# Kernel tuning notes

Measured on AMD Instinct MI355X. Metric: run time of the kernel, lower is better.

Reference implementation:

```python
import jax, jax.numpy as jnp
import numpy as np

B, N = 8192, 512
WEIGHT_THRESHOLD = 0.0
EPS = 1e-5


def setup_inputs() -> dict:
    key = jax.random.key(0)
    k1, k2, k3 = jax.random.split(key, 3)
    src_points = jax.random.normal(k1, (B, N, 3), dtype=jnp.float32)
    tgt_points = jax.random.normal(k2, (B, N, 3), dtype=jnp.float32)
    weights = jax.random.uniform(k3, (B, N), dtype=jnp.float32)
    return {"src_points": src_points, "tgt_points": tgt_points, "weights": weights}


def _weighted_procrustes(src, tgt, w):
    # threshold + normalize weights  (B, N)
    w = jnp.where(w < WEIGHT_THRESHOLD, jnp.zeros_like(w), w)
    w = w / (jnp.sum(w, axis=1, keepdims=True) + EPS)
    w3 = w[..., None]                                   # (B, N, 1)
    # weighted centroids (B, 1, 3)
    src_c = jnp.sum(w3 * src, axis=1, keepdims=True)
    tgt_c = jnp.sum(w3 * tgt, axis=1, keepdims=True)
    src0 = src - src_c
    tgt0 = tgt - tgt_c
    # weighted covariance H = src0^T (w * tgt0)  -> (B, 3, 3)
    H = jnp.einsum("bni,bnj->bij", src0, w3 * tgt0)
    U, S, Vh = jnp.linalg.svd(H)
    V = jnp.swapaxes(Vh, -1, -2)
    Ut = jnp.swapaxes(U, -1, -2)
    # reflection correction: diag(1, 1, sign(det(V U^T)))
    det = jnp.linalg.det(jnp.matmul(V, Ut))             # (B,)
    ones = jnp.ones((src.shape[0], 2), dtype=src.dtype)
    d = jnp.concatenate([ones, jnp.sign(det)[:, None]], axis=1)  # (B, 3)
    R = jnp.einsum("bij,bj,bjk->bik", V, d, Ut)         # (B, 3, 3)
    t = tgt_c[:, 0, :] - jnp.einsum("bij,bj->bi", R, src_c[:, 0, :])  # (B, 3)
    return R, t


def reference(src_points, tgt_points, weights):
    return _weighted_procrustes(src_points, tgt_points, weights)
```

## Files before the change

### kernel.cpp

```cpp
#include <hip/hip_runtime.h>

#define NPTS 512
#define BLOCK 256
#define XPS 68

#define GLOBAL_AS(p) ((const __attribute__((address_space(1))) void*)(p))
#define LDS_AS(p)    ((__attribute__((address_space(3))) void*)(p))

__global__ __launch_bounds__(BLOCK) void wproc_moments(
    const float* __restrict__ src,
    const float* __restrict__ tgt,
    const float* __restrict__ wts,
    float* __restrict__ ws)
{
    const int b = blockIdx.x;
    const int t = threadIdx.x;
    const int wave = t >> 6, lane = t & 63;

    __shared__ __align__(16) char smem[4 * 16 * XPS * 4];
    __shared__ float red[4][16];

    const char* sb = (const char*)(src + (size_t)b * (NPTS * 3));
    const char* tb = (const char*)(tgt + (size_t)b * (NPTS * 3));
    const char* wb = (const char*)(wts + (size_t)b * NPTS);

    for (int c = wave; c < 14; c += 4) {
        const char* g;
        if (c < 6)       g = sb + (size_t)c * 1024;
        else if (c < 12) g = tb + (size_t)(c - 6) * 1024;
        else             g = wb + (size_t)(c - 12) * 1024;
        __builtin_amdgcn_global_load_lds(
            GLOBAL_AS(g + lane * 16),
            LDS_AS(smem + c * 1024),
            16, 0, 2);
    }
    __syncthreads();

    const float* s_s = (const float*)smem;
    const float* s_t = (const float*)(smem + 6144);
    const float* s_w = (const float*)(smem + 12288);

    float acc[16];
    #pragma unroll
    for (int i = 0; i < 16; ++i) acc[i] = 0.f;

    #pragma unroll
    for (int k = 0; k < 2; ++k) {
        const int p = t + k * 256;
        float w = s_w[p];
        w = (w < 0.f) ? 0.f : w;
        const float sx = s_s[3 * p + 0], sy = s_s[3 * p + 1], sz = s_s[3 * p + 2];
        const float tx = s_t[3 * p + 0], ty = s_t[3 * p + 1], tz = s_t[3 * p + 2];
        acc[0] += w;
        acc[1] += w * sx; acc[2] += w * sy; acc[3] += w * sz;
        acc[4] += w * tx; acc[5] += w * ty; acc[6] += w * tz;
        const float wsx = w * sx, wsy = w * sy, wsz = w * sz;
        acc[7]  += wsx * tx; acc[8]  += wsx * ty; acc[9]  += wsx * tz;
        acc[10] += wsy * tx; acc[11] += wsy * ty; acc[12] += wsy * tz;
        acc[13] += wsz * tx; acc[14] += wsz * ty; acc[15] += wsz * tz;
    }
    __syncthreads();

    float (*xp)[16][XPS] = (float (*)[16][XPS])smem;
    #pragma unroll
    for (int m = 0; m < 16; ++m) xp[wave][m][lane] = acc[m];

    {
        const int m = lane & 15, q = lane >> 4;
        const float4* row = (const float4*)&xp[wave][m][0] + 4 * q;
        float4 a0 = row[0], a1 = row[1], a2 = row[2], a3 = row[3];
        a0.x += a1.x; a0.y += a1.y; a0.z += a1.z; a0.w += a1.w;
        a2.x += a3.x; a2.y += a3.y; a2.z += a3.z; a2.w += a3.w;
        a0.x += a2.x; a0.y += a2.y; a0.z += a2.z; a0.w += a2.w;
        float v = (a0.x + a0.y) + (a0.z + a0.w);
        v += __shfl_xor(v, 16, 64);
        v += __shfl_xor(v, 32, 64);
        if (q == 0) red[wave][m] = v;
    }
    __syncthreads();

    if (t < 16) {
        ws[(size_t)b * 16 + t] =
            (red[0][t] + red[1][t]) + (red[2][t] + red[3][t]);
    }
}

__global__ __launch_bounds__(BLOCK) void wproc_solve(
    const float* __restrict__ ws,
    float* __restrict__ out,
    int B)
{
    const int b = blockIdx.x * BLOCK + threadIdx.x;
    if (b >= B) return;

    double m[16];
    #pragma unroll
    for (int i = 0; i < 16; ++i) m[i] = (double)ws[(size_t)b * 16 + i];

    const double T = m[0] + 1e-5;
    const double f = 2.0 - m[0] / T;
    const double cs[3] = { m[1] / T, m[2] / T, m[3] / T };
    const double ct[3] = { m[4] / T, m[5] / T, m[6] / T };
    double H[3][3];
    for (int i = 0; i < 3; ++i)
        for (int j = 0; j < 3; ++j)
            H[i][j] = m[7 + i * 3 + j] / T - f * cs[i] * ct[j];

    double A[3][3];
    for (int i = 0; i < 3; ++i)
        for (int j = 0; j < 3; ++j)
            A[i][j] = H[0][i] * H[0][j] + H[1][i] * H[1][j] + H[2][i] * H[2][j];

    double V[3][3] = { {1, 0, 0}, {0, 1, 0}, {0, 0, 1} };
    for (int sweep = 0; sweep < 5; ++sweep) {
        for (int pair = 0; pair < 3; ++pair) {
            const int p = (pair == 2) ? 1 : 0;
            const int q = (pair == 0) ? 1 : 2;
            const double apq = A[p][q];
            if (apq == 0.0) continue;
            const double theta = (A[q][q] - A[p][p]) / (2.0 * apq);
            const double tt = ((theta >= 0.0) ? 1.0 : -1.0)
                            / (fabs(theta) + sqrt(theta * theta + 1.0));
            const double c = 1.0 / sqrt(tt * tt + 1.0);
            const double sn = tt * c;
            for (int k = 0; k < 3; ++k) {
                const double akp = A[k][p], akq = A[k][q];
                A[k][p] = c * akp - sn * akq;
                A[k][q] = sn * akp + c * akq;
            }
            for (int k = 0; k < 3; ++k) {
                const double apk = A[p][k], aqk = A[q][k];
                A[p][k] = c * apk - sn * aqk;
                A[q][k] = sn * apk + c * aqk;
            }
            for (int k = 0; k < 3; ++k) {
                const double vkp = V[k][p], vkq = V[k][q];
                V[k][p] = c * vkp - sn * vkq;
                V[k][q] = sn * vkp + c * vkq;
            }
        }
    }

    const double lam[3] = { A[0][0], A[1][1], A[2][2] };
    int i0 = 0, i1 = 1, i2 = 2;
    if (lam[i0] < lam[i1]) { int tmp = i0; i0 = i1; i1 = tmp; }
    if (lam[i0] < lam[i2]) { int tmp = i0; i0 = i2; i2 = tmp; }
    if (lam[i1] < lam[i2]) { int tmp = i1; i1 = i2; i2 = tmp; }

    const double v1[3] = { V[0][i0], V[1][i0], V[2][i0] };
    const double v2[3] = { V[0][i1], V[1][i1], V[2][i1] };
    const double v3[3] = { v1[1] * v2[2] - v1[2] * v2[1],
                           v1[2] * v2[0] - v1[0] * v2[2],
                           v1[0] * v2[1] - v1[1] * v2[0] };

    double u1[3], u2[3], u3[3];
    for (int i = 0; i < 3; ++i)
        u1[i] = H[i][0] * v1[0] + H[i][1] * v1[1] + H[i][2] * v1[2];
    double n1 = sqrt(u1[0] * u1[0] + u1[1] * u1[1] + u1[2] * u1[2]);
    n1 = (n1 > 1e-30) ? n1 : 1e-30;
    for (int i = 0; i < 3; ++i) u1[i] /= n1;

    for (int i = 0; i < 3; ++i)
        u2[i] = H[i][0] * v2[0] + H[i][1] * v2[1] + H[i][2] * v2[2];
    const double d12 = u1[0] * u2[0] + u1[1] * u2[1] + u1[2] * u2[2];
    for (int i = 0; i < 3; ++i) u2[i] -= d12 * u1[i];
    double n2 = sqrt(u2[0] * u2[0] + u2[1] * u2[1] + u2[2] * u2[2]);
    n2 = (n2 > 1e-30) ? n2 : 1e-30;
    for (int i = 0; i < 3; ++i) u2[i] /= n2;

    u3[0] = u1[1] * u2[2] - u1[2] * u2[1];
    u3[1] = u1[2] * u2[0] - u1[0] * u2[2];
    u3[2] = u1[0] * u2[1] - u1[1] * u2[0];

    double R[3][3];
    for (int i = 0; i < 3; ++i)
        for (int j = 0; j < 3; ++j)
            R[i][j] = v1[i] * u1[j] + v2[i] * u2[j] + v3[i] * u3[j];

    double tv[3];
    for (int i = 0; i < 3; ++i)
        tv[i] = ct[i] - (R[i][0] * cs[0] + R[i][1] * cs[1] + R[i][2] * cs[2]);

    float* outR = out + (size_t)b * 9;
    for (int i = 0; i < 3; ++i)
        for (int j = 0; j < 3; ++j)
            outR[i * 3 + j] = (float)R[i][j];
    float* outT = out + (size_t)B * 9 + (size_t)b * 3;
    for (int i = 0; i < 3; ++i) outT[i] = (float)tv[i];
}

extern "C" void kernel_launch(void* const* d_in, const int* in_sizes, int n_in,
                              void* d_out, int out_size, void* d_ws, size_t ws_size,
                              hipStream_t stream) {
    const float* src = (const float*)d_in[0];
    const float* tgt = (const float*)d_in[1];
    const float* wts = (const float*)d_in[2];
    float* out = (float*)d_out;
    float* ws = (float*)d_ws;
    const int B = out_size / 12;

    wproc_moments<<<B, BLOCK, 0, stream>>>(src, tgt, wts, ws);
    wproc_solve<<<(B + BLOCK - 1) / BLOCK, BLOCK, 0, stream>>>(ws, out, B);
}
```

Before: 143.5 us.

## Assign one batch element per wave and load points directly into registers

Each 64-lane wave now processes one full batch element, with four elements per block. Points are read with float4 loads straight into registers instead of being staged through LDS via global_load_lds. This removes the block-wide barriers and the cross-wave reduction step. It relies on wave-synchronous LDS access without explicit barriers and uses a strided float4 access pattern.

```diff
diff --git a/kernel.cpp b/kernel.cpp
--- a/kernel.cpp
+++ b/kernel.cpp
@@ -4,85 +4,78 @@
 #define BLOCK 256
 #define XPS 68
 
-#define GLOBAL_AS(p) ((const __attribute__((address_space(1))) void*)(p))
-#define LDS_AS(p)    ((__attribute__((address_space(3))) void*)(p))
-
 __global__ __launch_bounds__(BLOCK) void wproc_moments(
     const float* __restrict__ src,
     const float* __restrict__ tgt,
     const float* __restrict__ wts,
-    float* __restrict__ ws)
+    float* __restrict__ ws,
+    int B)
 {
-    const int b = blockIdx.x;
     const int t = threadIdx.x;
     const int wave = t >> 6, lane = t & 63;
+    const int b = blockIdx.x * 4 + wave;
 
-    __shared__ __align__(16) char smem[4 * 16 * XPS * 4];
-    __shared__ float red[4][16];
+    __shared__ __align__(16) float xp[4][16][XPS];
 
-    const char* sb = (const char*)(src + (size_t)b * (NPTS * 3));
-    const char* tb = (const char*)(tgt + (size_t)b * (NPTS * 3));
-    const char* wb = (const char*)(wts + (size_t)b * NPTS);
+    if (b >= B) return;
 
-    for (int c = wave; c < 14; c += 4) {
-        const char* g;
-        if (c < 6)       g = sb + (size_t)c * 1024;
-        else if (c < 12) g = tb + (size_t)(c - 6) * 1024;
-        else             g = wb + (size_t)(c - 12) * 1024;
-        __builtin_amdgcn_global_load_lds(
-            GLOBAL_AS(g + lane * 16),
-            LDS_AS(smem + c * 1024),
-            16, 0, 2);
-    }
-    __syncthreads();
+    const float4* sb = (const float4*)(src + (size_t)b * (NPTS * 3));
+    const float4* tb = (const float4*)(tgt + (size_t)b * (NPTS * 3));
+    const float4* wb = (const float4*)(wts + (size_t)b * NPTS);
 
-    const float* s_s = (const float*)smem;
-    const float* s_t = (const float*)(smem + 6144);
-    const float* s_w = (const float*)(smem + 12288);
+    const float4 w0  = wb[lane];
+    const float4 s0a = sb[3 * lane + 0];
+    const float4 s0b = sb[3 * lane + 1];
+    const float4 s0c = sb[3 * lane + 2];
+    const float4 t0a = tb[3 * lane + 0];
+    const float4 t0b = tb[3 * lane + 1];
+    const float4 t0c = tb[3 * lane + 2];
+    const float4 w1  = wb[lane + 64];
+    const float4 s1a = sb[3 * lane + 192];
+    const float4 s1b = sb[3 * lane + 193];
+    const float4 s1c = sb[3 * lane + 194];
+    const float4 t1a = tb[3 * lane + 192];
+    const float4 t1b = tb[3 * lane + 193];
+    const float4 t1c = tb[3 * lane + 194];
 
     float acc[16];
     #pragma unroll
     for (int i = 0; i < 16; ++i) acc[i] = 0.f;
 
-    #pragma unroll
-    for (int k = 0; k < 2; ++k) {
-        const int p = t + k * 256;
-        float w = s_w[p];
-        w = (w < 0.f) ? 0.f : w;
-        const float sx = s_s[3 * p + 0], sy = s_s[3 * p + 1], sz = s_s[3 * p + 2];
-        const float tx = s_t[3 * p + 0], ty = s_t[3 * p + 1], tz = s_t[3 * p + 2];
-        acc[0] += w;
-        acc[1] += w * sx; acc[2] += w * sy; acc[3] += w * sz;
-        acc[4] += w * tx; acc[5] += w * ty; acc[6] += w * tz;
-        const float wsx = w * sx, wsy = w * sy, wsz = w * sz;
-        acc[7]  += wsx * tx; acc[8]  += wsx * ty; acc[9]  += wsx * tz;
-        acc[10] += wsy * tx; acc[11] += wsy * ty; acc[12] += wsy * tz;
-        acc[13] += wsz * tx; acc[14] += wsz * ty; acc[15] += wsz * tz;
-    }
-    __syncthreads();
+    #define ACC_PT(w_, sx, sy, sz, tx, ty, tz) do {                          \
+        const float w = ((w_) < 0.f) ? 0.f : (w_);   \
+        acc[0] += w;                                                          \
+        acc[1] += w * (sx); acc[2] += w * (sy); acc[3] += w * (sz);           \
+        acc[4] += w * (tx); acc[5] += w * (ty); acc[6] += w * (tz);           \
+        const float wsx = w * (sx), wsy = w * (sy), wsz = w * (sz);           \
+        acc[7]  += wsx * (tx); acc[8]  += wsx * (ty); acc[9]  += wsx * (tz);  \
+        acc[10] += wsy * (tx); acc[11] += wsy * (ty); acc[12] += wsy * (tz);  \
+        acc[13] += wsz * (tx); acc[14] += wsz * (ty); acc[15] += wsz * (tz);  \
+    } while (0)
 
-    float (*xp)[16][XPS] = (float (*)[16][XPS])smem;
+    ACC_PT(w0.x, s0a.x, s0a.y, s0a.z, t0a.x, t0a.y, t0a.z);
+    ACC_PT(w0.y, s0a.w, s0b.x, s0b.y, t0a.w, t0b.x, t0b.y);
+    ACC_PT(w0.z, s0b.z, s0b.w, s0c.x, t0b.z, t0b.w, t0c.x);
+    ACC_PT(w0.w, s0c.y, s0c.z, s0c.w, t0c.y, t0c.z, t0c.w);
+    ACC_PT(w1.x, s1a.x, s1a.y, s1a.z, t1a.x, t1a.y, t1a.z);
+    ACC_PT(w1.y, s1a.w, s1b.x, s1b.y, t1a.w, t1b.x, t1b.y);
+    ACC_PT(w1.z, s1b.z, s1b.w, s1c.x, t1b.z, t1b.w, t1c.x);
+    ACC_PT(w1.w, s1c.y, s1c.z, s1c.w, t1c.y, t1c.z, t1c.w);
+    #undef ACC_PT
+
     #pragma unroll
     for (int m = 0; m < 16; ++m) xp[wave][m][lane] = acc[m];
 
-    {
-        const int m = lane & 15, q = lane >> 4;
-        const float4* row = (const float4*)&xp[wave][m][0] + 4 * q;
-        float4 a0 = row[0], a1 = row[1], a2 = row[2], a3 = row[3];
-        a0.x += a1.x; a0.y += a1.y; a0.z += a1.z; a0.w += a1.w;
-        a2.x += a3.x; a2.y += a3.y; a2.z += a3.z; a2.w += a3.w;
-        a0.x += a2.x; a0.y += a2.y; a0.z += a2.z; a0.w += a2.w;
-        float v = (a0.x + a0.y) + (a0.z + a0.w);
-        v += __shfl_xor(v, 16, 64);
-        v += __shfl_xor(v, 32, 64);
-        if (q == 0) red[wave][m] = v;
-    }
-    __syncthreads();
-
-    if (t < 16) {
-        ws[(size_t)b * 16 + t] =
-            (red[0][t] + red[1][t]) + (red[2][t] + red[3][t]);
-    }
+    const int m = lane & 15, q = lane >> 4;
+    const float4* row = (const float4*)&xp[wave][m][0] + 4 * q;
+    float4 a0 = row[0], a1 = row[1], a2 = row[2], a3 = row[3];
+    a0.x += a1.x; a0.y += a1.y; a0.z += a1.z; a0.w += a1.w;
+    a2.x += a3.x; a2.y += a3.y; a2.z += a3.z; a2.w += a3.w;
+    a0.x += a2.x; a0.y += a2.y; a0.z += a2.z; a0.w += a2.w;
+    float v = (a0.x + a0.y) + (a0.z + a0.w);
+    v += __shfl_xor(v, 16, 64);
+    v += __shfl_xor(v, 32, 64);
+    if (q == 0) ws[(size_t)b * 16 + m] = v;
 }
 
 __global__ __launch_bounds__(BLOCK) void wproc_solve(
@@ -199,6 +192,6 @@
     float* ws = (float*)d_ws;
     const int B = out_size / 12;
 
-    wproc_moments<<<B, BLOCK, 0, stream>>>(src, tgt, wts, ws);
+    wproc_moments<<<(B + 3) / 4, BLOCK, 0, stream>>>(src, tgt, wts, ws, B);
     wproc_solve<<<(B + BLOCK - 1) / BLOCK, BLOCK, 0, stream>>>(ws, out, B);
 }
```

After: 149.6 us. 1.04x slower.
